# Kernel tuning notes

Measured on AMD Instinct MI355X. Metric: run time of the kernel, lower is better.

## Reference

```python
import jax, jax.numpy as jnp
import numpy as np

N_QUBITS = 8      # kernel_size == n wires
N_LAYERS = 4
OUT_CHANNELS = 8
STRIDE = 1


def _ry(state, theta, wire):
    """Apply RY(theta) on `wire`. state: (P, 2,2,...,2) real; theta scalar or (P,)."""
    axis = wire + 1
    a0 = jnp.take(state, 0, axis=axis)
    a1 = jnp.take(state, 1, axis=axis)
    half = theta * 0.5
    c, s = jnp.cos(half), jnp.sin(half)
    # broadcast per-patch angles over remaining qubit axes
    extra = a0.ndim - jnp.ndim(c)
    if extra > 0:
        c = jnp.reshape(c, jnp.shape(c) + (1,) * extra)
        s = jnp.reshape(s, jnp.shape(s) + (1,) * extra)
    return jnp.stack([c * a0 - s * a1, s * a0 + c * a1], axis=axis)


def _cnot(state, ctrl, tgt):
    ca, ta = ctrl + 1, tgt + 1
    c0 = jnp.take(state, 0, axis=ca)
    c1 = jnp.take(state, 1, axis=ca)
    ta_adj = ta - 1 if ta > ca else ta  # target axis index after removing ctrl axis
    c1 = jnp.flip(c1, axis=ta_adj)      # X on target where ctrl==1
    return jnp.stack([c0, c1], axis=ca)


def _circuit(patches, w):
    """Batched statevector simulation. patches: (P, N_QUBITS); w: (N_LAYERS*N_QUBITS,).
    RY/CNOT on a real |0...0> keep the state real -> float32 statevector."""
    P = patches.shape[0]
    state = jnp.zeros((P,) + (2,) * N_QUBITS, dtype=patches.dtype)
    state = state.at[(slice(None),) + (0,) * N_QUBITS].set(1.0)
    # AngleEmbedding: RY(pi * x_q) on wire q
    for q in range(N_QUBITS):
        state = _ry(state, patches[:, q] * jnp.pi, q)
    for layer in range(N_LAYERS):
        for q in range(N_QUBITS):
            state = _ry(state, w[layer * N_QUBITS + q], q)
        for q in range(N_QUBITS - 1):
            state = _cnot(state, q, q + 1)
    # <Z x Z x ... x Z> = sum |amp|^2 * (-1)^parity(bits)
    z = jnp.array([1.0, -1.0], dtype=state.dtype)
    sign = z
    for _ in range(N_QUBITS - 1):
        sign = sign[..., None] * z
    return jnp.sum(state * state * sign, axis=tuple(range(1, N_QUBITS + 1)))


def setup_inputs() -> dict:
    key = jax.random.key(0)
    k1, k2 = jax.random.split(key)
    x = jax.random.uniform(k1, (128, 1, 512), dtype=jnp.float32)
    weights = jax.random.uniform(k2, (OUT_CHANNELS, N_LAYERS * N_QUBITS), dtype=jnp.float32) * (2.0 * jnp.pi)
    return {"x": x, "weights": weights}


def reference(x, weights):
    B, _, L = x.shape
    out_L = (L - N_QUBITS) // STRIDE + 1
    # gather all sliding-window patches at once: (B, out_L, K) -> (B*out_L, K)
    idx = jnp.arange(out_L)[:, None] * STRIDE + jnp.arange(N_QUBITS)[None, :]
    patches = x[:, 0, idx].reshape(B * out_L, N_QUBITS)
    outs = [_circuit(patches, weights[k]) for k in range(OUT_CHANNELS)]
    out = jnp.stack(outs, axis=0).reshape(OUT_CHANNELS, B, out_L)
    return jnp.transpose(out, (1, 0, 2))  # (B, C_out, out_L)
```

## Files before the change

kernel.cpp:

```cpp
#include <hip/hip_runtime.h>
#include <math.h>

#define NQ       8
#define NLAYERS  4
#define OUTC     8
#define BATCH    128
#define LEN      512
#define OUTL     505
#define NPATCH   (BATCH * OUTL)
#define BM       64
#define NBLK     (NPATCH / BM)
#define BLK_PER_CH 1010

typedef __attribute__((ext_vector_type(8))) short bf16x8;
typedef __attribute__((ext_vector_type(4))) float f32x4;

__device__ __forceinline__ ushort to_bf16(float f) {
    union { float f; unsigned int u; } v; v.f = f;
    unsigned int b = v.u + 0x7FFFu + ((v.u >> 16) & 1u);
    return (ushort)(b >> 16);
}

__device__ __forceinline__ unsigned pk_bf16(float lo, float hi) {
    unsigned r;
    asm("v_cvt_pk_bf16_f32 %0, %1, %2" : "=v"(r) : "v"(lo), "v"(hi));
    return r;
}

template <int CTRL>
__device__ __forceinline__ float dpp_xor(float x) {
    int i = __float_as_int(x);
    int r = __builtin_amdgcn_update_dpp(0, i, CTRL, 0xF, 0xF, true);
    return __int_as_float(r);
}

template <int N>
__device__ __forceinline__ float ror_add(float x) {
    int i = __float_as_int(x);
    int r = __builtin_amdgcn_update_dpp(0, i, 0x120 + N, 0xF, 0xF, true);
    return x + __int_as_float(r);
}

__device__ __forceinline__ void run_layers(float st[64], const float* wk, int b0, int b7) {
#pragma unroll 1
    for (int layer = 0; layer < NLAYERS; ++layer) {
        float wc[NQ], wsn[NQ];
#pragma unroll
        for (int q = 0; q < NQ; ++q) {
            float half = 0.5f * wk[layer * NQ + q];
            wc[q]  = __cosf(half);
            wsn[q] = __sinf(half);
        }
        {
            const float sg = b0 ? wsn[0] : -wsn[0];
#pragma unroll
            for (int r = 0; r < 64; ++r) {
                float p = dpp_xor<0x4E>(st[r]);
                st[r] = fmaf(wc[0], st[r], sg * p);
            }
        }
#pragma unroll
        for (int q = 1; q <= 6; ++q) {
            const int m = 1 << (6 - q);
#pragma unroll
            for (int r = 0; r < 64; ++r) {
                if (r & m) continue;
                float a0 = st[r], a1 = st[r + m];
                st[r]     = fmaf(wc[q], a0, -wsn[q] * a1);
                st[r + m] = fmaf(wc[q], a1,  wsn[q] * a0);
            }
        }
        {
            const float sg = b7 ? wsn[7] : -wsn[7];
#pragma unroll
            for (int r = 0; r < 64; ++r) {
                float p = dpp_xor<0xB1>(st[r]);
                st[r] = fmaf(wc[7], st[r], sg * p);
            }
        }
#pragma unroll
        for (int r = 0; r < 32; ++r) {
            float t0 = st[r], t1 = st[r + 32];
            st[r]      = b0 ? t1 : t0;
            st[r + 32] = b0 ? t0 : t1;
        }
#pragma unroll
        for (int q = 1; q <= 5; ++q) {
            const int cm = 1 << (6 - q);
            const int tm = 1 << (5 - q);
#pragma unroll
            for (int r = 0; r < 64; ++r) {
                if ((r & cm) && !(r & tm)) {
                    float t = st[r]; st[r] = st[r + tm]; st[r + tm] = t;
                }
            }
        }
#pragma unroll
        for (int r = 1; r < 64; r += 2) st[r] = dpp_xor<0xB1>(st[r]);
    }
}

__global__ __launch_bounds__(256) void build_m(const float* __restrict__ w,
                                               ushort* __restrict__ W2) {
    const int tid  = threadIdx.x;
    const int lane = tid & 63;
    const int k    = blockIdx.x >> 2;
    const int j    = ((blockIdx.x & 3) << 6) | (tid >> 2);
    const int b0 = (lane >> 1) & 1;
    const int b7 = lane & 1;

    float st[64];
    const int r0 = (j >> 1) & 63;
    const bool mine = (b0 == ((j >> 7) & 1)) && (b7 == (j & 1));
#pragma unroll
    for (int r = 0; r < 64; ++r) st[r] = (mine && r == r0) ? 1.0f : 0.0f;

    run_layers(st, w + k * (NLAYERS * NQ), b0, b7);

    const int ph = (k << 3) | (j >> 5);
    const int gj = (j >> 3) & 3;
    const int je = j & 7;
#pragma unroll
    for (int r = 0; r < 64; ++r) {
        int i  = (b0 << 7) | (r << 1) | b7;
        size_t idx = (size_t)((ph * 4 + (i >> 6)) * 4 + ((i >> 4) & 3)) * 512
                   + (gj * 16 + (i & 15)) * 8 + je;
        W2[idx] = to_bf16(st[r]);
    }
}

__global__ __launch_bounds__(256, 2) void qconv_mfma(const float* __restrict__ x,
                                                     const ushort* __restrict__ W2,
                                                     float* __restrict__ out) {
    __shared__ ushort Alds[64 * 256];
    __shared__ float  red[OUTC * 4 * 64];

    const int tid  = threadIdx.x;
    const int lane = tid & 63;
    const int wv   = tid >> 6;
    const int u    = lane & 15;
    const int g    = lane >> 4;
    const int pbase = blockIdx.x * BM;
    const int c0   = blockIdx.x & 7;

    const ushort* bbase = W2 + (size_t)wv * 2048 + lane * 8;

    uint4 breg[4];
#pragma unroll
    for (int ct = 0; ct < 4; ++ct)
        breg[ct] = *(const uint4*)(bbase + (size_t)c0 * 65536 + ct * 512);

    {
        const int row = lane;
        const int jb  = wv;
        const int p = pbase + row;
        const int b = p / OUTL, ol = p - b * OUTL;
        const float* xp = x + b * LEN + ol;
        float ec[NQ], es[NQ];
#pragma unroll
        for (int q = 0; q < NQ; ++q) {
            float half = xp[q] * 1.5707963267948966f;
            ec[q] = __cosf(half);
            es[q] = __sinf(half);
        }
        float st[64];
        st[0] = (jb & 2 ? es[0] : ec[0]) * (jb & 1 ? es[1] : ec[1]);
#pragma unroll
        for (int q = 2; q <= 7; ++q) {
            const int m = 1 << (7 - q);
#pragma unroll
            for (int jj = (1 << (q - 2)) - 1; jj >= 0; --jj) {
                float v = st[jj * 2 * m];
                st[jj * 2 * m + m] = v * es[q];
                st[jj * 2 * m]     = v * ec[q];
            }
        }
#pragma unroll
        for (int cc = 0; cc < 8; ++cc) {
            uint4 vv;
            vv.x = pk_bf16(st[cc * 8 + 0], st[cc * 8 + 1]);
            vv.y = pk_bf16(st[cc * 8 + 2], st[cc * 8 + 3]);
            vv.z = pk_bf16(st[cc * 8 + 4], st[cc * 8 + 5]);
            vv.w = pk_bf16(st[cc * 8 + 6], st[cc * 8 + 7]);
            int phys = ((jb * 8 + cc) ^ (row & 7)) & 31;
            *(uint4*)((char*)Alds + row * 512 + phys * 16) = vv;
        }
    }
    __syncthreads();

    const int pu = __builtin_popcount(u) & 1;
    const int pw = __builtin_popcount(wv) & 1;
    const float slane = ((pu ^ pw) & 1) ? -1.0f : 1.0f;

#pragma unroll 1
    for (int it = 0; it < 8; ++it) {
        const int c  = (it + c0) & 7;
        const int cn = (it + 1 + c0) & 7;

        f32x4 acc[4][4];
#pragma unroll
        for (int a = 0; a < 4; ++a)
#pragma unroll
            for (int cq = 0; cq < 4; ++cq) acc[a][cq] = (f32x4){0.f, 0.f, 0.f, 0.f};

#pragma unroll
        for (int s = 0; s < 8; ++s) {
#pragma unroll
            for (int rt = 0; rt < 4; ++rt) {
                int row = rt * 16 + u;
                int phys = ((s * 4 + g) ^ (row & 7)) & 31;
                bf16x8 af = *(const bf16x8*)((const char*)Alds + row * 512 + phys * 16);
#pragma unroll
                for (int ct = 0; ct < 4; ++ct)
                    acc[rt][ct] = __builtin_amdgcn_mfma_f32_16x16x32_bf16(
                        af, *(bf16x8*)&breg[ct], acc[rt][ct], 0, 0, 0);
            }
            const int phn = (s < 7) ? (c * 8 + s + 1) : (cn * 8);
            if (!(it == 7 && s == 7)) {
#pragma unroll
                for (int ct = 0; ct < 4; ++ct)
                    breg[ct] = *(const uint4*)(bbase + (size_t)phn * 8192 + ct * 512);
            }
        }

#pragma unroll
        for (int rt = 0; rt < 4; ++rt) {
            f32x4 pe = acc[rt][0] * acc[rt][0];
            pe += acc[rt][3] * acc[rt][3];
            f32x4 po = acc[rt][1] * acc[rt][1];
            po += acc[rt][2] * acc[rt][2];
            f32x4 part = (pe - po) * slane;
            float v0 = part[0], v1 = part[1], v2 = part[2], v3 = part[3];
            v0 = ror_add<8>(ror_add<4>(ror_add<2>(ror_add<1>(v0))));
            v1 = ror_add<8>(ror_add<4>(ror_add<2>(ror_add<1>(v1))));
            v2 = ror_add<8>(ror_add<4>(ror_add<2>(ror_add<1>(v2))));
            v3 = ror_add<8>(ror_add<4>(ror_add<2>(ror_add<1>(v3))));
            if (u == 0) {
                f32x4 vv = (f32x4){v0, v1, v2, v3};
                *(f32x4*)&red[(c * 4 + wv) * 64 + rt * 16 + g * 4] = vv;
            }
        }
    }

    __syncthreads();
#pragma unroll
    for (int e = 0; e < 2; ++e) {
        int idx = tid + e * 256;
        int ch = idx >> 6, row = idx & 63;
        float o = red[(ch * 4 + 0) * 64 + row] + red[(ch * 4 + 1) * 64 + row] +
                  red[(ch * 4 + 2) * 64 + row] + red[(ch * 4 + 3) * 64 + row];
        int p = pbase + row;
        int b = p / OUTL, ol = p - b * OUTL;
        out[b * (OUTC * OUTL) + ch * OUTL + ol] = o;
    }
}

__global__ __launch_bounds__(256) void qconv_direct(const float* __restrict__ x,
                                                    const float* __restrict__ w,
                                                    float* __restrict__ out) {
    const int lane = threadIdx.x & 63;
    const int wave = threadIdx.x >> 6;
    const int bi   = blockIdx.x;
    const int k    = bi / BLK_PER_CH;
    const int pblk = bi % BLK_PER_CH;
    const int patch = pblk * 64 + wave * 16 + (lane >> 2);
    const int b0 = (lane >> 1) & 1;
    const int b7 = lane & 1;
    const int b  = patch / OUTL;
    const int ol = patch - b * OUTL;
    const float* xp = x + b * LEN + ol;

    float ec[NQ], es[NQ];
#pragma unroll
    for (int q = 0; q < NQ; ++q) {
        float half = xp[q] * 1.5707963267948966f;
        ec[q] = __cosf(half);
        es[q] = __sinf(half);
    }
    float st[64];
    st[0] = (b0 ? es[0] : ec[0]) * (b7 ? es[7] : ec[7]);
#pragma unroll
    for (int q = 1; q <= 6; ++q) {
        const int m = 1 << (6 - q);
#pragma unroll
        for (int j = (1 << (q - 1)) - 1; j >= 0; --j) {
            float v = st[j * 2 * m];
            st[j * 2 * m + m] = v * es[q];
            st[j * 2 * m]     = v * ec[q];
        }
    }
    run_layers(st, w + k * (NLAYERS * NQ), b0, b7);

    float accp = 0.0f, accm = 0.0f;
#pragma unroll
    for (int r = 0; r < 64; ++r) {
        if (__builtin_popcount(r) & 1) accm = fmaf(st[r], st[r], accm);
        else                           accp = fmaf(st[r], st[r], accp);
    }
    float v = accp - accm;
    if (b0 ^ b7) v = -v;
    v += dpp_xor<0xB1>(v);
    v += dpp_xor<0x4E>(v);
    if ((lane & 3) == 0) out[b * (OUTC * OUTL) + k * OUTL + ol] = v;
}

extern "C" void kernel_launch(void* const* d_in, const int* in_sizes, int n_in,
                              void* d_out, int out_size, void* d_ws, size_t ws_size,
                              hipStream_t stream) {
    const float* x = (const float*)d_in[0];
    const float* w = (const float*)d_in[1];
    float* out = (float*)d_out;

    if (ws_size < (size_t)(8 * 256 * 256 * 2)) {
        qconv_direct<<<dim3(OUTC * BLK_PER_CH), 256, 0, stream>>>(x, w, out);
        return;
    }
    ushort* W2 = (ushort*)d_ws;
    build_m<<<dim3(32), 256, 0, stream>>>(w, W2);
    qconv_mfma<<<dim3(NBLK), 256, 0, stream>>>(x, W2, out);
}
```

Measured before the change: 82.99 us.

## Split output channels across two blocks per patch tile in MFMA kernel

Each 64-patch tile is now handled by two blocks, each covering four of the eight output channels instead of all eight. The grid doubles from 1010 to 2020 blocks, which gives the GPU more blocks to keep compute units busy and shortens each block's serial channel loop. The cost is that the patch state preparation (trig evaluation, state build, bf16 packing into LDS) is now done twice per tile. The shared reduction buffer is halved as well.

```diff
diff --git a/kernel.cpp b/kernel.cpp
--- a/kernel.cpp
+++ b/kernel.cpp
@@ -133,22 +133,25 @@
                                                      const ushort* __restrict__ W2,
                                                      float* __restrict__ out) {
     __shared__ ushort Alds[64 * 256];
-    __shared__ float  red[OUTC * 4 * 64];
+    __shared__ float  red[4 * 4 * 64];
 
     const int tid  = threadIdx.x;
     const int lane = tid & 63;
     const int wv   = tid >> 6;
     const int u    = lane & 15;
     const int g    = lane >> 4;
-    const int pbase = blockIdx.x * BM;
-    const int c0   = blockIdx.x & 7;
+    const int bid  = blockIdx.x;
+    const int pblk = bid >> 1;
+    const int cb   = (bid & 1) * 4;
+    const int pbase = pblk * BM;
+    const int c0   = pblk & 3;
 
     const ushort* bbase = W2 + (size_t)wv * 2048 + lane * 8;
 
     uint4 breg[4];
 #pragma unroll
     for (int ct = 0; ct < 4; ++ct)
-        breg[ct] = *(const uint4*)(bbase + (size_t)c0 * 65536 + ct * 512);
+        breg[ct] = *(const uint4*)(bbase + (size_t)(cb + c0) * 65536 + ct * 512);
 
     {
         const int row = lane;
@@ -193,9 +196,9 @@
     const float slane = ((pu ^ pw) & 1) ? -1.0f : 1.0f;
 
 #pragma unroll 1
-    for (int it = 0; it < 8; ++it) {
-        const int c  = (it + c0) & 7;
-        const int cn = (it + 1 + c0) & 7;
+    for (int it = 0; it < 4; ++it) {
+        const int c  = cb + ((it + c0) & 3);
+        const int cn = cb + ((it + 1 + c0) & 3);
 
         f32x4 acc[4][4];
 #pragma unroll
@@ -216,7 +219,7 @@
                         af, *(bf16x8*)&breg[ct], acc[rt][ct], 0, 0, 0);
             }
             const int phn = (s < 7) ? (c * 8 + s + 1) : (cn * 8);
-            if (!(it == 7 && s == 7)) {
+            if (!(it == 3 && s == 7)) {
 #pragma unroll
                 for (int ct = 0; ct < 4; ++ct)
                     breg[ct] = *(const uint4*)(bbase + (size_t)phn * 8192 + ct * 512);
@@ -237,18 +240,17 @@
             v3 = ror_add<8>(ror_add<4>(ror_add<2>(ror_add<1>(v3))));
             if (u == 0) {
                 f32x4 vv = (f32x4){v0, v1, v2, v3};
-                *(f32x4*)&red[(c * 4 + wv) * 64 + rt * 16 + g * 4] = vv;
+                *(f32x4*)&red[((c & 3) * 4 + wv) * 64 + rt * 16 + g * 4] = vv;
             }
         }
     }
 
     __syncthreads();
-#pragma unroll
-    for (int e = 0; e < 2; ++e) {
-        int idx = tid + e * 256;
-        int ch = idx >> 6, row = idx & 63;
-        float o = red[(ch * 4 + 0) * 64 + row] + red[(ch * 4 + 1) * 64 + row] +
-                  red[(ch * 4 + 2) * 64 + row] + red[(ch * 4 + 3) * 64 + row];
+    {
+        int chl = tid >> 6, row = tid & 63;
+        int ch = cb + chl;
+        float o = red[(chl * 4 + 0) * 64 + row] + red[(chl * 4 + 1) * 64 + row] +
+                  red[(chl * 4 + 2) * 64 + row] + red[(chl * 4 + 3) * 64 + row];
         int p = pbase + row;
         int b = p / OUTL, ol = p - b * OUTL;
         out[b * (OUTC * OUTL) + ch * OUTL + ol] = o;
@@ -317,5 +319,5 @@
     }
     ushort* W2 = (ushort*)d_ws;
     build_m<<<dim3(32), 256, 0, stream>>>(w, W2);
-    qconv_mfma<<<dim3(NBLK), 256, 0, stream>>>(x, W2, out);
-}
+    qconv_mfma<<<dim3(NBLK * 2), 256, 0, stream>>>(x, W2, out);
+}
```

Measured after the change: 81.06 us (median of 3 runs). 1.02x faster.
